# Performance work log

Hardware: AMD Instinct MI355X
Metric: run time of the kernel (lower is better)

## Reference

```python
import jax, jax.numpy as jnp
import numpy as np

N, P, Q, T, J, B, H = 262144, 64, 64, 2048, 512, 8, 64


def setup_inputs() -> dict:
    key = jax.random.key(0)
    ks = jax.random.split(key, 11)
    sH = 1.0 / np.sqrt(H).astype(np.float32)
    return {
        "idx": jax.random.randint(ks[0], (B,), 0, J),
        "seg_ids": jnp.sort(jax.random.randint(ks[1], (N,), 0, T)),
        "K": jax.random.normal(ks[2], (N, P), jnp.float32) * 0.1,
        "V": jax.random.normal(ks[3], (N, Q), jnp.float32),
        "S": jax.random.normal(ks[4], (P, J), jnp.float32) * 0.1,
        "W_ih": jax.random.normal(ks[5], (3 * H, Q), jnp.float32) * sH,
        "W_hh": jax.random.normal(ks[6], (3 * H, H), jnp.float32) * sH,
        "b_ih": jax.random.normal(ks[7], (3 * H,), jnp.float32) * sH,
        "b_hh": jax.random.normal(ks[8], (3 * H,), jnp.float32) * sH,
        "w_out": jax.random.normal(ks[9], (1, H), jnp.float32) * sH,
        "b_out": jax.random.normal(ks[10], (1,), jnp.float32) * sH,
    }


def reference(idx, seg_ids, K, V, S, W_ih, W_hh, b_ih, b_hh, w_out, b_out):
    # W[:, b] = K @ S[:, idx[b]]  -> [N, B]
    w = K @ S[:, idx]
    # ragged per-segment softmax over the N axis (segments = date windows)
    m = jax.ops.segment_max(w, seg_ids, num_segments=T)          # [T, B]
    e = jnp.exp(w - m[seg_ids])                                  # [N, B]
    denom = jax.ops.segment_sum(e, seg_ids, num_segments=T)     # [T, B]
    alpha = e / denom[seg_ids]                                   # [N, B]
    # weighted aggregation of V rows per segment: M[t, b] = sum_u alpha_u * V_u
    M = jax.ops.segment_sum(alpha[:, :, None] * V[:, None, :],
                            seg_ids, num_segments=T)             # [T, B, Q]
    X = jnp.transpose(M, (1, 0, 2))                              # [B, T, Q]

    # PyTorch GRU (gate order r,z,n). Faithful to the original bug: GRU was
    # built without batch_first=True, so axis 0 (B) is time, axis 1 (T) is batch.
    def step(h, x_t):  # x_t: [T, Q], h: [T, H]
        gi = x_t @ W_ih.T + b_ih                                 # [T, 3H]
        gh = h @ W_hh.T + b_hh                                   # [T, 3H]
        i_r, i_z, i_n = jnp.split(gi, 3, axis=1)
        h_r, h_z, h_n = jnp.split(gh, 3, axis=1)
        r = jax.nn.sigmoid(i_r + h_r)
        z = jax.nn.sigmoid(i_z + h_z)
        n = jnp.tanh(i_n + r * h_n)
        h_new = (1.0 - z) * n + z * h
        return h_new, h_new

    h0 = jnp.zeros((T, H), X.dtype)
    _, hs = jax.lax.scan(step, h0, X)                            # [B, T, H]
    preds = hs @ w_out.T + b_out                                 # [B, T, 1]
    return preds
```

## Files before the change

### kernel.cpp

```cpp
#include <hip/hip_runtime.h>
#include <math.h>

#define NN 262144
#define PP 64
#define QQ 64
#define TT 2048
#define JJ 512
#define BB 8
#define HH 64
#define PSTRIDE 520

__device__ __forceinline__ float lane_bcast(float v, int l) {
  return __int_as_float(__builtin_amdgcn_readlane(__float_as_int(v), l));
}

__global__ __launch_bounds__(256) void k_wp(const float* __restrict__ Kmat,
                                            const int* __restrict__ idx,
                                            const float* __restrict__ S,
                                            const int* __restrict__ seg_ids,
                                            float* __restrict__ ew,
                                            int* __restrict__ seg_start) {
  int tid = threadIdx.x;
  int gtid = blockIdx.x * 256 + tid;
  if (gtid <= TT) {
    int lo = 0, hi = NN;
    while (lo < hi) {
      int mid = (lo + hi) >> 1;
      if (seg_ids[mid] < gtid) lo = mid + 1; else hi = mid;
    }
    seg_start[gtid] = lo;
  }
  __shared__ __align__(16) float s_lds[BB * PP];
  for (int i = tid; i < BB * PP; i += 256) {
    int p = i >> 3, b = i & 7;
    s_lds[b * PP + p] = S[p * JJ + idx[b]];
  }
  __syncthreads();
  int n = blockIdx.x * 64 + (tid >> 2);
  int sub = tid & 3;
  const float4* Kp = reinterpret_cast<const float4*>(Kmat + (size_t)n * PP + sub * 16);
  float4 kq[4];
#pragma unroll
  for (int j = 0; j < 4; ++j) kq[j] = Kp[j];
  float acc[8];
#pragma unroll
  for (int b = 0; b < 8; ++b) acc[b] = 0.f;
#pragma unroll
  for (int j4 = 0; j4 < 4; ++j4) {
    float4 kk = kq[j4];
#pragma unroll
    for (int b = 0; b < 8; ++b) {
      const float4 sv = *reinterpret_cast<const float4*>(&s_lds[b * PP + sub * 16 + j4 * 4]);
      acc[b] += kk.x * sv.x + kk.y * sv.y + kk.z * sv.z + kk.w * sv.w;
    }
  }
#pragma unroll
  for (int b = 0; b < 8; ++b) {
    acc[b] += __shfl_xor(acc[b], 1);
    acc[b] += __shfl_xor(acc[b], 2);
  }
  float ox = (sub == 0) ? acc[0] : (sub == 1) ? acc[2] : (sub == 2) ? acc[4] : acc[6];
  float oy = (sub == 0) ? acc[1] : (sub == 1) ? acc[3] : (sub == 2) ? acc[5] : acc[7];
  reinterpret_cast<float2*>(ew + (size_t)n * 8)[sub] =
      make_float2(__expf(ox), __expf(oy));
}

__global__ __launch_bounds__(256) void k_segp(const float* __restrict__ ew,
                                              const float* __restrict__ V,
                                              const int* __restrict__ seg_start,
                                              float* __restrict__ P) {
  int lane = threadIdx.x & 63, j = threadIdx.x >> 6;
  int t = blockIdx.x;
  int s = seg_start[t], e = seg_start[t + 1];
  int len = e - s;
  int chunk = (len + 3) >> 2;
  int b0 = s + j * chunk;
  int b1 = b0 + chunk; if (b1 > e) b1 = e;
  int slen = (b1 > b0) ? (b1 - b0) : 0;
  int rsub = lane >> 4;
  int qg = lane & 15;

  float4 acc[8];
#pragma unroll
  for (int b = 0; b < 8; ++b) acc[b] = make_float4(0.f, 0.f, 0.f, 0.f);
  float4 selo = make_float4(0.f, 0.f, 0.f, 0.f);
  float4 sehi = make_float4(0.f, 0.f, 0.f, 0.f);

#define PROC(RR)                                                                                           \
  {                                                                                                        \
    int r_ = (RR);                                                                                         \
    const float4* ewp_ = reinterpret_cast<const float4*>(ew + (size_t)r_ * 8);                             \
    float4 elo = ewp_[0], ehi = ewp_[1];                                                                   \
    float4 vv = reinterpret_cast<const float4*>(V + (size_t)r_ * QQ)[qg];                                  \
    selo.x += elo.x; selo.y += elo.y; selo.z += elo.z; selo.w += elo.w;                                    \
    sehi.x += ehi.x; sehi.y += ehi.y; sehi.z += ehi.z; sehi.w += ehi.w;                                    \
    acc[0].x += elo.x * vv.x; acc[0].y += elo.x * vv.y; acc[0].z += elo.x * vv.z; acc[0].w += elo.x * vv.w; \
    acc[1].x += elo.y * vv.x; acc[1].y += elo.y * vv.y; acc[1].z += elo.y * vv.z; acc[1].w += elo.y * vv.w; \
    acc[2].x += elo.z * vv.x; acc[2].y += elo.z * vv.y; acc[2].z += elo.z * vv.z; acc[2].w += elo.z * vv.w; \
    acc[3].x += elo.w * vv.x; acc[3].y += elo.w * vv.y; acc[3].z += elo.w * vv.z; acc[3].w += elo.w * vv.w; \
    acc[4].x += ehi.x * vv.x; acc[4].y += ehi.x * vv.y; acc[4].z += ehi.x * vv.z; acc[4].w += ehi.x * vv.w; \
    acc[5].x += ehi.y * vv.x; acc[5].y += ehi.y * vv.y; acc[5].z += ehi.y * vv.z; acc[5].w += ehi.y * vv.w; \
    acc[6].x += ehi.z * vv.x; acc[6].y += ehi.z * vv.y; acc[6].z += ehi.z * vv.z; acc[6].w += ehi.z * vv.w; \
    acc[7].x += ehi.w * vv.x; acc[7].y += ehi.w * vv.y; acc[7].z += ehi.w * vv.z; acc[7].w += ehi.w * vv.w; \
  }

  int nfull = slen >> 2, tail = slen & 3;
  for (int i = 0; i < nfull; ++i) PROC(b0 + i * 4 + rsub);
  if (tail && rsub < tail) PROC(b0 + nfull * 4 + rsub);
#undef PROC

#pragma unroll
  for (int b = 0; b < 8; ++b) {
    acc[b].x += __shfl_xor(acc[b].x, 16); acc[b].y += __shfl_xor(acc[b].y, 16);
    acc[b].z += __shfl_xor(acc[b].z, 16); acc[b].w += __shfl_xor(acc[b].w, 16);
    acc[b].x += __shfl_xor(acc[b].x, 32); acc[b].y += __shfl_xor(acc[b].y, 32);
    acc[b].z += __shfl_xor(acc[b].z, 32); acc[b].w += __shfl_xor(acc[b].w, 32);
  }
  selo.x += __shfl_xor(selo.x, 16); selo.y += __shfl_xor(selo.y, 16);
  selo.z += __shfl_xor(selo.z, 16); selo.w += __shfl_xor(selo.w, 16);
  sehi.x += __shfl_xor(sehi.x, 16); sehi.y += __shfl_xor(sehi.y, 16);
  sehi.z += __shfl_xor(sehi.z, 16); sehi.w += __shfl_xor(sehi.w, 16);
  selo.x += __shfl_xor(selo.x, 32); selo.y += __shfl_xor(selo.y, 32);
  selo.z += __shfl_xor(selo.z, 32); selo.w += __shfl_xor(selo.w, 32);
  sehi.x += __shfl_xor(sehi.x, 32); sehi.y += __shfl_xor(sehi.y, 32);
  sehi.z += __shfl_xor(sehi.z, 32); sehi.w += __shfl_xor(sehi.w, 32);

  float* Pp = P + ((size_t)t * 4 + j) * PSTRIDE;
  if (rsub == 0) {
#pragma unroll
    for (int b = 0; b < 8; ++b)
      *reinterpret_cast<float4*>(Pp + b * 64 + qg * 4) = acc[b];
    if (qg == 0) {
      Pp[512] = selo.x; Pp[513] = selo.y; Pp[514] = selo.z; Pp[515] = selo.w;
      Pp[516] = sehi.x; Pp[517] = sehi.y; Pp[518] = sehi.z; Pp[519] = sehi.w;
    }
  }
}

__global__ __launch_bounds__(256) void k_gir(const float* __restrict__ P,
                                             const float* __restrict__ W_ih,
                                             const float* __restrict__ b_ih,
                                             float* __restrict__ GI) {
  __shared__ float Wt[64 * 193];
  int tid = threadIdx.x;
  for (int i = tid; i < 192 * 64; i += 256) {
    int g = i >> 6, k = i & 63;
    Wt[k * 193 + g] = W_ih[i];
  }
  __syncthreads();
  int lane = tid & 63, wv = tid >> 6;
  int row0 = blockIdx.x * 32 + wv * 8;
  float x[8];
#pragma unroll
  for (int rr = 0; rr < 8; ++rr) {
    int rho = row0 + rr;
    int b = rho >> 11, t = rho & 2047;
    const float* P0 = P + (size_t)t * 4 * PSTRIDE;
    float dd = P0[512 + b] + P0[PSTRIDE + 512 + b] +
               P0[2 * PSTRIDE + 512 + b] + P0[3 * PSTRIDE + 512 + b];
    float inv = (dd > 0.f) ? 1.f / dd : 0.f;
    float sum = P0[b * 64 + lane] + P0[PSTRIDE + b * 64 + lane] +
                P0[2 * PSTRIDE + b * 64 + lane] + P0[3 * PSTRIDE + b * 64 + lane];
    x[rr] = sum * inv;
  }
  float bi0 = b_ih[lane], bi1 = b_ih[64 + lane], bi2 = b_ih[128 + lane];
  float a0[8], a1[8], a2[8];
#pragma unroll
  for (int rr = 0; rr < 8; ++rr) { a0[rr] = bi0; a1[rr] = bi1; a2[rr] = bi2; }
#pragma unroll
  for (int k = 0; k < 64; ++k) {
    float w0 = Wt[k * 193 + lane];
    float w1 = Wt[k * 193 + 64 + lane];
    float w2 = Wt[k * 193 + 128 + lane];
#pragma unroll
    for (int rr = 0; rr < 8; ++rr) {
      float xk = lane_bcast(x[rr], k);
      a0[rr] += w0 * xk; a1[rr] += w1 * xk; a2[rr] += w2 * xk;
    }
  }
#pragma unroll
  for (int rr = 0; rr < 8; ++rr) {
    size_t rho = (size_t)row0 + rr;
    GI[rho * 192 + lane]       = a0[rr];
    GI[rho * 192 + 64 + lane]  = a1[rr];
    GI[rho * 192 + 128 + lane] = a2[rr];
  }
}

__global__ __launch_bounds__(256) void k_gru(const float* __restrict__ GI,
                                             const float* __restrict__ W_hh,
                                             const float* __restrict__ b_hh,
                                             const float* __restrict__ w_out,
                                             const float* __restrict__ b_out,
                                             float* __restrict__ preds) {
  __shared__ __align__(16) float Wl[192 * 68];
  int tid = threadIdx.x;
  for (int i = tid; i < 192 * 16; i += 256) {
    int g = i >> 4, c = i & 15;
    *reinterpret_cast<float4*>(&Wl[g * 68 + c * 4]) =
        *reinterpret_cast<const float4*>(W_hh + g * 64 + c * 4);
  }
  __syncthreads();
  int lane = tid & 63, wv = tid >> 6;
  int t = blockIdx.x * 4 + wv;
  float bh0 = b_hh[lane], bh1 = b_hh[64 + lane], bh2 = b_hh[128 + lane];
  float wo = w_out[lane];
  float bo = b_out[0];
  const float* w0base = &Wl[lane * 68];
  const float* w1base = &Wl[(64 + lane) * 68];
  const float* w2base = &Wl[(128 + lane) * 68];

  float gr[8], gz[8], gn[8];
#pragma unroll
  for (int b = 0; b < 8; ++b) {
    size_t base = ((size_t)b * TT + t) * 192;
    gr[b] = GI[base + lane];
    gz[b] = GI[base + 64 + lane];
    gn[b] = GI[base + 128 + lane];
  }

  float h;
  {
    float r = 1.f / (1.f + __expf(-(gr[0] + bh0)));
    float z = 1.f / (1.f + __expf(-(gz[0] + bh1)));
    float nv = tanhf(gn[0] + r * bh2);
    h = (1.f - z) * nv;
    float pv = h * wo;
#pragma unroll
    for (int off = 32; off; off >>= 1) pv += __shfl_xor(pv, off);
    if (lane == 0) preds[t] = pv + bo;
  }
#pragma unroll
  for (int b = 1; b < 8; ++b) {
    float ar = bh0, az = bh1, an = bh2;
#pragma unroll
    for (int c = 0; c < 16; ++c) {
      const float4 w0 = *reinterpret_cast<const float4*>(w0base + c * 4);
      const float4 w1 = *reinterpret_cast<const float4*>(w1base + c * 4);
      const float4 w2 = *reinterpret_cast<const float4*>(w2base + c * 4);
      float a0 = lane_bcast(h, c * 4 + 0), a1 = lane_bcast(h, c * 4 + 1);
      float a2 = lane_bcast(h, c * 4 + 2), a3 = lane_bcast(h, c * 4 + 3);
      ar += w0.x * a0 + w0.y * a1 + w0.z * a2 + w0.w * a3;
      az += w1.x * a0 + w1.y * a1 + w1.z * a2 + w1.w * a3;
      an += w2.x * a0 + w2.y * a1 + w2.z * a2 + w2.w * a3;
    }
    float r = 1.f / (1.f + __expf(-(gr[b] + ar)));
    float z = 1.f / (1.f + __expf(-(gz[b] + az)));
    float nv = tanhf(gn[b] + r * an);
    h = (1.f - z) * nv + z * h;
    float pv = h * wo;
#pragma unroll
    for (int off = 32; off; off >>= 1) pv += __shfl_xor(pv, off);
    if (lane == 0) preds[(size_t)b * TT + t] = pv + bo;
  }
}

extern "C" void kernel_launch(void* const* d_in, const int* in_sizes, int n_in,
                              void* d_out, int out_size, void* d_ws, size_t ws_size,
                              hipStream_t stream) {
  const int*   idx     = (const int*)d_in[0];
  const int*   seg_ids = (const int*)d_in[1];
  const float* Kmat    = (const float*)d_in[2];
  const float* V       = (const float*)d_in[3];
  const float* S       = (const float*)d_in[4];
  const float* W_ih    = (const float*)d_in[5];
  const float* W_hh    = (const float*)d_in[6];
  const float* b_ih    = (const float*)d_in[7];
  const float* b_hh    = (const float*)d_in[8];
  const float* w_out   = (const float*)d_in[9];
  const float* b_out   = (const float*)d_in[10];
  float* out = (float*)d_out;

  char* ws = (char*)d_ws;
  int*   seg_start = (int*)(ws + 0);
  float* ew = (float*)(ws + 8448);
  float* P  = (float*)(ws + 8397056);
  float* GI = (float*)(ws + 25434112);

  hipLaunchKernelGGL(k_wp, dim3(NN / 64), dim3(256), 0, stream,
                     Kmat, idx, S, seg_ids, ew, seg_start);
  hipLaunchKernelGGL(k_segp, dim3(TT), dim3(256), 0, stream, ew, V, seg_start, P);
  hipLaunchKernelGGL(k_gir, dim3(512), dim3(256), 0, stream, P, W_ih, b_ih, GI);
  hipLaunchKernelGGL(k_gru, dim3(512), dim3(256), 0, stream, GI, W_hh, b_hh, w_out, b_out, out);
}
```

Measured before the change: 75.52 us.

## Split segment aggregation into fixed row-block partials plus per-segment reduction kernel

Replaces the one-block-per-segment weighted aggregation with fixed 32-row blocks. Each block masks rows by segment, reduces over lanes and waves, and writes partial sums into up to seven slots per segment. A new reduction kernel sums the slots, applies the softmax normalisation and writes a dense M, which the input-gate GEMM then reads directly. The aim is even work per block regardless of segment length. The cost is extra partial-sum traffic to and from global memory and one more launch. It also assumes each 32-row block touches at most two segments and each segment spans at most seven blocks.

```diff
diff --git a/kernel.cpp b/kernel.cpp
--- a/kernel.cpp
+++ b/kernel.cpp
@@ -8,7 +8,8 @@
 #define JJ 512
 #define BB 8
 #define HH 64
-#define PSTRIDE 520
+#define NSLOT 7
+#define PSTR 520
 
 __device__ __forceinline__ float lane_bcast(float v, int l) {
   return __int_as_float(__builtin_amdgcn_readlane(__float_as_int(v), l));
@@ -65,82 +66,138 @@
       make_float2(__expf(ox), __expf(oy));
 }
 
-__global__ __launch_bounds__(256) void k_segp(const float* __restrict__ ew,
+__global__ __launch_bounds__(256) void k_segB(const float* __restrict__ ew,
                                               const float* __restrict__ V,
+                                              const int* __restrict__ seg_ids,
                                               const int* __restrict__ seg_start,
-                                              float* __restrict__ P) {
-  int lane = threadIdx.x & 63, j = threadIdx.x >> 6;
-  int t = blockIdx.x;
+                                              float* __restrict__ P3) {
+  __shared__ int seg_lds[32];
+  __shared__ int slot_lds;
+  __shared__ __align__(16) float accred[4][8][64];
+  __shared__ float reds[4][8];
+  int tid = threadIdx.x;
+  int n0 = blockIdx.x * 32;
+  if (tid < 32) seg_lds[tid] = seg_ids[n0 + tid];
+  __syncthreads();
+  int t_lo = seg_lds[0], t_hi = seg_lds[31];
+  if (tid == 0) slot_lds = (int)blockIdx.x - (seg_start[t_lo] >> 5);
+
+  int lane = tid & 63, w = tid >> 6;
+  int rsub = lane >> 4, qg = lane & 15;
+  int rA = w * 8 + rsub;
+  int rB = rA + 4;
+  int tA = seg_lds[rA], tB = seg_lds[rB];
+
+  const float4* ePA = reinterpret_cast<const float4*>(ew + (size_t)(n0 + rA) * 8);
+  const float4* ePB = reinterpret_cast<const float4*>(ew + (size_t)(n0 + rB) * 8);
+  float4 eloA = ePA[0], ehiA = ePA[1];
+  float4 eloB = ePB[0], ehiB = ePB[1];
+  float4 vvA = reinterpret_cast<const float4*>(V + (size_t)(n0 + rA) * QQ)[qg];
+  float4 vvB = reinterpret_cast<const float4*>(V + (size_t)(n0 + rB) * QQ)[qg];
+
+#define PASS(TSEL, SLOT)                                                                                   \
+  {                                                                                                        \
+    float wA = (tA == (TSEL)) ? 1.f : 0.f;                                                                 \
+    float wB = (tB == (TSEL)) ? 1.f : 0.f;                                                                 \
+    float4 la = make_float4(eloA.x * wA, eloA.y * wA, eloA.z * wA, eloA.w * wA);                           \
+    float4 ha = make_float4(ehiA.x * wA, ehiA.y * wA, ehiA.z * wA, ehiA.w * wA);                           \
+    float4 lb = make_float4(eloB.x * wB, eloB.y * wB, eloB.z * wB, eloB.w * wB);                           \
+    float4 hb = make_float4(ehiB.x * wB, ehiB.y * wB, ehiB.z * wB, ehiB.w * wB);                           \
+    float4 acc[8];                                                                                         \
+    acc[0] = make_float4(la.x * vvA.x + lb.x * vvB.x, la.x * vvA.y + lb.x * vvB.y,                         \
+                         la.x * vvA.z + lb.x * vvB.z, la.x * vvA.w + lb.x * vvB.w);                        \
+    acc[1] = make_float4(la.y * vvA.x + lb.y * vvB.x, la.y * vvA.y + lb.y * vvB.y,                         \
+                         la.y * vvA.z + lb.y * vvB.z, la.y * vvA.w + lb.y * vvB.w);                        \
+    acc[2] = make_float4(la.z * vvA.x + lb.z * vvB.x, la.z * vvA.y + lb.z * vvB.y,                         \
+                         la.z * vvA.z + lb.z * vvB.z, la.z * vvA.w + lb.z * vvB.w);                        \
+    acc[3] = make_float4(la.w * vvA.x + lb.w * vvB.x, la.w * vvA.y + lb.w * vvB.y,                         \
+                         la.w * vvA.z + lb.w * vvB.z, la.w * vvA.w + lb.w * vvB.w);                        \
+    acc[4] = make_float4(ha.x * vvA.x + hb.x * vvB.x, ha.x * vvA.y + hb.x * vvB.y,                         \
+                         ha.x * vvA.z + hb.x * vvB.z, ha.x * vvA.w + hb.x * vvB.w);                        \
+    acc[5] = make_float4(ha.y * vvA.x + hb.y * vvB.x, ha.y * vvA.y + hb.y * vvB.y,                         \
+                         ha.y * vvA.z + hb.y * vvB.z, ha.y * vvA.w + hb.y * vvB.w);                        \
+    acc[6] = make_float4(ha.z * vvA.x + hb.z * vvB.x, ha.z * vvA.y + hb.z * vvB.y,                         \
+                         ha.z * vvA.z + hb.z * vvB.z, ha.z * vvA.w + hb.z * vvB.w);                        \
+    acc[7] = make_float4(ha.w * vvA.x + hb.w * vvB.x, ha.w * vvA.y + hb.w * vvB.y,                         \
+                         ha.w * vvA.z + hb.w * vvB.z, ha.w * vvA.w + hb.w * vvB.w);                        \
+    float se[8] = {la.x + lb.x, la.y + lb.y, la.z + lb.z, la.w + lb.w,                                     \
+                   ha.x + hb.x, ha.y + hb.y, ha.z + hb.z, ha.w + hb.w};                                    \
+    _Pragma("unroll")                                                                                      \
+    for (int b = 0; b < 8; ++b) {                                                                          \
+      acc[b].x += __shfl_xor(acc[b].x, 16); acc[b].y += __shfl_xor(acc[b].y, 16);                          \
+      acc[b].z += __shfl_xor(acc[b].z, 16); acc[b].w += __shfl_xor(acc[b].w, 16);                          \
+      acc[b].x += __shfl_xor(acc[b].x, 32); acc[b].y += __shfl_xor(acc[b].y, 32);                          \
+      acc[b].z += __shfl_xor(acc[b].z, 32); acc[b].w += __shfl_xor(acc[b].w, 32);                          \
+      se[b] += __shfl_xor(se[b], 16);                                                                      \
+      se[b] += __shfl_xor(se[b], 32);                                                                      \
+    }                                                                                                      \
+    if (rsub == 0) {                                                                                       \
+      _Pragma("unroll")                                                                                    \
+      for (int b = 0; b < 8; ++b)                                                                          \
+        *reinterpret_cast<float4*>(&accred[w][b][qg * 4]) = acc[b];                                        \
+      if (qg == 0) {                                                                                       \
+        _Pragma("unroll")                                                                                  \
+        for (int b = 0; b < 8; ++b) reds[w][b] = se[b];                                                    \
+      }                                                                                                    \
+    }                                                                                                      \
+    __syncthreads();                                                                                       \
+    {                                                                                                      \
+      float* Pp = P3 + ((size_t)(TSEL) * NSLOT + (SLOT)) * PSTR;                                           \
+      for (int o = tid; o < 512; o += 256) {                                                               \
+        int b = o >> 6, q = o & 63;                                                                        \
+        Pp[o] = accred[0][b][q] + accred[1][b][q] + accred[2][b][q] + accred[3][b][q];                     \
+      }                                                                                                    \
+      if (tid < 8)                                                                                         \
+        Pp[512 + tid] = reds[0][tid] + reds[1][tid] + reds[2][tid] + reds[3][tid];                         \
+    }                                                                                                      \
+  }
+
+  __syncthreads();
+  int slot_lo = slot_lds;
+  PASS(t_lo, slot_lo);
+  if (t_lo != t_hi) {
+    __syncthreads();
+    PASS(t_hi, 0);
+  }
+#undef PASS
+}
+
+__global__ __launch_bounds__(256) void k_red(const float* __restrict__ P3,
+                                             const int* __restrict__ seg_start,
+                                             float* __restrict__ M) {
+  __shared__ float invL[8];
+  int t = blockIdx.x, tid = threadIdx.x;
   int s = seg_start[t], e = seg_start[t + 1];
-  int len = e - s;
-  int chunk = (len + 3) >> 2;
-  int b0 = s + j * chunk;
-  int b1 = b0 + chunk; if (b1 > e) b1 = e;
-  int slen = (b1 > b0) ? (b1 - b0) : 0;
-  int rsub = lane >> 4;
-  int qg = lane & 15;
-
-  float4 acc[8];
-#pragma unroll
-  for (int b = 0; b < 8; ++b) acc[b] = make_float4(0.f, 0.f, 0.f, 0.f);
-  float4 selo = make_float4(0.f, 0.f, 0.f, 0.f);
-  float4 sehi = make_float4(0.f, 0.f, 0.f, 0.f);
-
-#define PROC(RR)                                                                                           \
-  {                                                                                                        \
-    int r_ = (RR);                                                                                         \
-    const float4* ewp_ = reinterpret_cast<const float4*>(ew + (size_t)r_ * 8);                             \
-    float4 elo = ewp_[0], ehi = ewp_[1];                                                                   \
-    float4 vv = reinterpret_cast<const float4*>(V + (size_t)r_ * QQ)[qg];                                  \
-    selo.x += elo.x; selo.y += elo.y; selo.z += elo.z; selo.w += elo.w;                                    \
-    sehi.x += ehi.x; sehi.y += ehi.y; sehi.z += ehi.z; sehi.w += ehi.w;                                    \
-    acc[0].x += elo.x * vv.x; acc[0].y += elo.x * vv.y; acc[0].z += elo.x * vv.z; acc[0].w += elo.x * vv.w; \
-    acc[1].x += elo.y * vv.x; acc[1].y += elo.y * vv.y; acc[1].z += elo.y * vv.z; acc[1].w += elo.y * vv.w; \
-    acc[2].x += elo.z * vv.x; acc[2].y += elo.z * vv.y; acc[2].z += elo.z * vv.z; acc[2].w += elo.z * vv.w; \
-    acc[3].x += elo.w * vv.x; acc[3].y += elo.w * vv.y; acc[3].z += elo.w * vv.z; acc[3].w += elo.w * vv.w; \
-    acc[4].x += ehi.x * vv.x; acc[4].y += ehi.x * vv.y; acc[4].z += ehi.x * vv.z; acc[4].w += ehi.x * vv.w; \
-    acc[5].x += ehi.y * vv.x; acc[5].y += ehi.y * vv.y; acc[5].z += ehi.y * vv.z; acc[5].w += ehi.y * vv.w; \
-    acc[6].x += ehi.z * vv.x; acc[6].y += ehi.z * vv.y; acc[6].z += ehi.z * vv.z; acc[6].w += ehi.z * vv.w; \
-    acc[7].x += ehi.w * vv.x; acc[7].y += ehi.w * vv.y; acc[7].z += ehi.w * vv.z; acc[7].w += ehi.w * vv.w; \
-  }
-
-  int nfull = slen >> 2, tail = slen & 3;
-  for (int i = 0; i < nfull; ++i) PROC(b0 + i * 4 + rsub);
-  if (tail && rsub < tail) PROC(b0 + nfull * 4 + rsub);
-#undef PROC
-
-#pragma unroll
-  for (int b = 0; b < 8; ++b) {
-    acc[b].x += __shfl_xor(acc[b].x, 16); acc[b].y += __shfl_xor(acc[b].y, 16);
-    acc[b].z += __shfl_xor(acc[b].z, 16); acc[b].w += __shfl_xor(acc[b].w, 16);
-    acc[b].x += __shfl_xor(acc[b].x, 32); acc[b].y += __shfl_xor(acc[b].y, 32);
-    acc[b].z += __shfl_xor(acc[b].z, 32); acc[b].w += __shfl_xor(acc[b].w, 32);
-  }
-  selo.x += __shfl_xor(selo.x, 16); selo.y += __shfl_xor(selo.y, 16);
-  selo.z += __shfl_xor(selo.z, 16); selo.w += __shfl_xor(selo.w, 16);
-  sehi.x += __shfl_xor(sehi.x, 16); sehi.y += __shfl_xor(sehi.y, 16);
-  sehi.z += __shfl_xor(sehi.z, 16); sehi.w += __shfl_xor(sehi.w, 16);
-  selo.x += __shfl_xor(selo.x, 32); selo.y += __shfl_xor(selo.y, 32);
-  selo.z += __shfl_xor(selo.z, 32); selo.w += __shfl_xor(selo.w, 32);
-  sehi.x += __shfl_xor(sehi.x, 32); sehi.y += __shfl_xor(sehi.y, 32);
-  sehi.z += __shfl_xor(sehi.z, 32); sehi.w += __shfl_xor(sehi.w, 32);
-
-  float* Pp = P + ((size_t)t * 4 + j) * PSTRIDE;
-  if (rsub == 0) {
-#pragma unroll
-    for (int b = 0; b < 8; ++b)
-      *reinterpret_cast<float4*>(Pp + b * 64 + qg * 4) = acc[b];
-    if (qg == 0) {
-      Pp[512] = selo.x; Pp[513] = selo.y; Pp[514] = selo.z; Pp[515] = selo.w;
-      Pp[516] = sehi.x; Pp[517] = sehi.y; Pp[518] = sehi.z; Pp[519] = sehi.w;
-    }
-  }
-}
-
-__global__ __launch_bounds__(256) void k_gir(const float* __restrict__ P,
-                                             const float* __restrict__ W_ih,
-                                             const float* __restrict__ b_ih,
-                                             float* __restrict__ GI) {
+  int b0 = s >> 5;
+  int nb = (e > s) ? (((e - 1) >> 5) - b0 + 1) : 0;
+  if (tid < 8) {
+    float dd = 0.f;
+#pragma unroll
+    for (int jb = 0; jb < NSLOT; ++jb) {
+      int jc = (jb < nb) ? jb : 0;
+      float v = P3[((size_t)t * NSLOT + jc) * PSTR + 512 + tid];
+      dd += (jb < nb) ? v : 0.f;
+    }
+    invL[tid] = (dd > 0.f) ? 1.f / dd : 0.f;
+  }
+  __syncthreads();
+  for (int o = tid; o < 512; o += 256) {
+    int b = o >> 6;
+    float sum = 0.f;
+#pragma unroll
+    for (int jb = 0; jb < NSLOT; ++jb) {
+      int jc = (jb < nb) ? jb : 0;
+      float v = P3[((size_t)t * NSLOT + jc) * PSTR + o];
+      sum += (jb < nb) ? v : 0.f;
+    }
+    M[(size_t)t * 512 + o] = sum * invL[b];
+  }
+}
+
+__global__ __launch_bounds__(256) void k_gi(const float* __restrict__ M,
+                                            const float* __restrict__ W_ih,
+                                            const float* __restrict__ b_ih,
+                                            float* __restrict__ GI) {
   __shared__ float Wt[64 * 193];
   int tid = threadIdx.x;
   for (int i = tid; i < 192 * 64; i += 256) {
@@ -155,13 +212,7 @@
   for (int rr = 0; rr < 8; ++rr) {
     int rho = row0 + rr;
     int b = rho >> 11, t = rho & 2047;
-    const float* P0 = P + (size_t)t * 4 * PSTRIDE;
-    float dd = P0[512 + b] + P0[PSTRIDE + 512 + b] +
-               P0[2 * PSTRIDE + 512 + b] + P0[3 * PSTRIDE + 512 + b];
-    float inv = (dd > 0.f) ? 1.f / dd : 0.f;
-    float sum = P0[b * 64 + lane] + P0[PSTRIDE + b * 64 + lane] +
-                P0[2 * PSTRIDE + b * 64 + lane] + P0[3 * PSTRIDE + b * 64 + lane];
-    x[rr] = sum * inv;
+    x[rr] = M[((size_t)t * 8 + b) * 64 + lane];
   }
   float bi0 = b_ih[lane], bi1 = b_ih[64 + lane], bi2 = b_ih[128 + lane];
   float a0[8], a1[8], a2[8];
@@ -274,12 +325,15 @@
   char* ws = (char*)d_ws;
   int*   seg_start = (int*)(ws + 0);
   float* ew = (float*)(ws + 8448);
-  float* P  = (float*)(ws + 8397056);
-  float* GI = (float*)(ws + 25434112);
+  float* M  = (float*)(ws + 8397056);
+  float* P3 = (float*)(ws + 12591360);
+  float* GI = (float*)(ws + 12591360);
 
   hipLaunchKernelGGL(k_wp, dim3(NN / 64), dim3(256), 0, stream,
                      Kmat, idx, S, seg_ids, ew, seg_start);
-  hipLaunchKernelGGL(k_segp, dim3(TT), dim3(256), 0, stream, ew, V, seg_start, P);
-  hipLaunchKernelGGL(k_gir, dim3(512), dim3(256), 0, stream, P, W_ih, b_ih, GI);
+  hipLaunchKernelGGL(k_segB, dim3(NN / 32), dim3(256), 0, stream,
+                     ew, V, seg_ids, seg_start, P3);
+  hipLaunchKernelGGL(k_red, dim3(TT), dim3(256), 0, stream, P3, seg_start, M);
+  hipLaunchKernelGGL(k_gi, dim3(512), dim3(256), 0, stream, M, W_ih, b_ih, GI);
   hipLaunchKernelGGL(k_gru, dim3(512), dim3(256), 0, stream, GI, W_hh, b_hh, w_out, b_out, out);
 }
```

Result: slower. 112.6 us (+49.1%).
